# Performance work log

Measured on AMD Instinct MI355X. Metric: run time of the kernel, lower is better.

Reference implementation:

```python
import jax, jax.numpy as jnp
import numpy as np
from jax import lax

B, N, C, HEADS, SR = 2, 4096, 256, 8, 2
HW = 64

def setup_inputs() -> dict:
    key = jax.random.key(0)
    ks = jax.random.split(key, 12)
    s = 0.02
    return {
        "x0": jax.random.normal(ks[0], (B, N, C), jnp.float32),
        "x1": jax.random.normal(ks[1], (B, N, C), jnp.float32),
        "Wq": jax.random.normal(ks[2], (C, C), jnp.float32) * s,
        "Wkv": jax.random.normal(ks[3], (2 * C, C), jnp.float32) * s,
        "Wproj": jax.random.normal(ks[4], (C, C), jnp.float32) * s,
        "bproj": jnp.zeros((C,), jnp.float32),
        "Wsr": jax.random.normal(ks[5], (C, C, SR, SR), jnp.float32) * np.sqrt(2.0 / (SR * SR * C)),
        "bsr": jnp.zeros((C,), jnp.float32),
        "ln_w0": jnp.ones((C,), jnp.float32),
        "ln_b0": jnp.zeros((C,), jnp.float32),
        "ln_w1": jnp.ones((C,), jnp.float32),
        "ln_b1": jnp.zeros((C,), jnp.float32),
        "H": HW,
        "W": HW,
    }

def _layernorm(x, w, b, eps=1e-5):
    mu = jnp.mean(x, axis=-1, keepdims=True)
    var = jnp.mean(jnp.square(x - mu), axis=-1, keepdims=True)
    return (x - mu) * lax.rsqrt(var + eps) * w + b

def _attend(x, ln_w, ln_b, Wq, Wkv, Wproj, bproj, Wsr, bsr, H, W):
    b, n, c = x.shape
    h = HEADS
    d = c // h
    scale = d ** -0.5
    # q: (B, h, N, d)
    q = (x @ Wq.T).reshape(b, n, h, d).transpose(0, 2, 1, 3)
    # spatial reduction: conv k=stride=sr on (B,C,H,W)
    xs = x.transpose(0, 2, 1).reshape(b, c, H, W)
    xs = lax.conv_general_dilated(xs, Wsr, (SR, SR), 'VALID',
                                  dimension_numbers=('NCHW', 'OIHW', 'NCHW'))
    xs = xs + bsr[None, :, None, None]
    m = (H // SR) * (W // SR)
    xs = xs.reshape(b, c, m).transpose(0, 2, 1)  # (B, M, C)
    xs = _layernorm(xs, ln_w, ln_b)
    kv = (xs @ Wkv.T).reshape(b, m, 2, h, d).transpose(2, 0, 3, 1, 4)
    k, v = kv[0], kv[1]  # (B, h, M, d)
    attn = jnp.einsum('bhnd,bhmd->bhnm', q, k) * scale
    attn = jax.nn.softmax(attn, axis=-1)
    out = jnp.einsum('bhnm,bhmd->bhnd', attn, v)
    out = out.transpose(0, 2, 1, 3).reshape(b, n, c)
    return out @ Wproj.T + bproj

def reference(x0, x1, Wq, Wkv, Wproj, bproj, Wsr, bsr, ln_w0, ln_b0, ln_w1, ln_b1, H, W):
    y0 = _attend(x0, ln_w0, ln_b0, Wq, Wkv, Wproj, bproj, Wsr, bsr, H, W)
    y1 = _attend(x1, ln_w1, ln_b1, Wq, Wkv, Wproj, bproj, Wsr, bsr, H, W)
    return (y0, y1)
```

## Files before the change

kernel.cpp:

```cpp
#include <hip/hip_runtime.h>
#include <hip/hip_bf16.h>
#include <cstddef>

typedef __hip_bfloat16 bf16;
typedef __attribute__((ext_vector_type(8))) short bf16x8;
typedef __attribute__((ext_vector_type(4))) float f32x4;
typedef __attribute__((ext_vector_type(4))) short short4v;

__device__ __forceinline__ float b2f(bf16 v) { return __bfloat162float(v); }
__device__ __forceinline__ bf16 f2b(float v) { return __float2bfloat16(v); }

#define MFMA(a, b, c) __builtin_amdgcn_mfma_f32_16x16x32_bf16((a), (b), (c), 0, 0, 0)

#define WQ_OFF   0
#define WKV_OFF  65536
#define WP_OFF   196608
#define WSR_OFF  262144

__global__ __launch_bounds__(256) void cvt_x(
    const float* __restrict__ x0, const float* __restrict__ x1,
    bf16* __restrict__ xb) {
  const int gid = blockIdx.x * 256 + threadIdx.x;
  for (int i = gid; i < 1048576; i += 262144) {
    const float4 v = (i < 524288) ? ((const float4*)x0)[i]
                                  : ((const float4*)x1)[i - 524288];
    union { bf16 h[4]; short4v s; } u;
    u.h[0] = f2b(v.x); u.h[1] = f2b(v.y); u.h[2] = f2b(v.z); u.h[3] = f2b(v.w);
    ((short4v*)xb)[i] = u.s;
  }
}

__global__ __launch_bounds__(256) void cvt_w(
    const float* __restrict__ Wq, const float* __restrict__ Wkv,
    const float* __restrict__ Wp, const float* __restrict__ Wsr,
    bf16* __restrict__ wb) {
  const int gid = blockIdx.x * 256 + threadIdx.x;
  for (int i = gid; i < 524288; i += 131072) {
    float v;
    if (i < WKV_OFF)       v = Wq[i];
    else if (i < WP_OFF)   v = Wkv[i - WKV_OFF];
    else if (i < WSR_OFF)  v = Wp[i - WP_OFF];
    else {
      const int r = i - WSR_OFF;
      const int o = r >> 10, k = r & 1023;
      const int p = k >> 8, c = k & 255;
      v = Wsr[o * 1024 + c * 4 + p];
    }
    wb[i] = f2b(v);
  }
}

#define STAGE_W(W_lds, wgl, ldg)                                             \
  _Pragma("unroll")                                                          \
  for (int u = 0; u < 8; ++u) {                                              \
    const int idx = u * 256 + t;                                             \
    const int wr = idx >> 5;                                                 \
    const int wc = (idx & 31) * 8;                                           \
    *(bf16x8*)&W_lds[wr][wc] = *(const bf16x8*)((wgl) + wr * (ldg) + wc);    \
  }

__global__ __launch_bounds__(256) void qproj_mfma(
    const bf16* __restrict__ xb, const bf16* __restrict__ wb,
    bf16* __restrict__ q) {
  __shared__ bf16 W_lds[64][264];
  const int t = threadIdx.x;
  const int wave = t >> 6, lane = t & 63, quad = lane >> 4, l16 = lane & 15;
  const int row0 = blockIdx.x * 64 + wave * 16;
  const int colh = blockIdx.y * 64;
  STAGE_W(W_lds, wb + WQ_OFF + colh * 256, 256);
  __syncthreads();
  const bf16* ap = xb + (row0 + l16) * 256 + quad * 8;
  f32x4 acc[4];
  #pragma unroll
  for (int j = 0; j < 4; ++j) acc[j] = (f32x4){0.f, 0.f, 0.f, 0.f};
  #pragma unroll
  for (int k0 = 0; k0 < 256; k0 += 32) {
    const bf16x8 af = *(const bf16x8*)(ap + k0);
    #pragma unroll
    for (int j = 0; j < 4; ++j) {
      const bf16x8 wf = *(const bf16x8*)&W_lds[j * 16 + l16][k0 + quad * 8];
      acc[j] = MFMA(af, wf, acc[j]);
    }
  }
  const float scale = 0.17677669529663687f;
  #pragma unroll
  for (int j = 0; j < 4; ++j)
    #pragma unroll
    for (int r = 0; r < 4; ++r)
      q[(row0 + quad * 4 + r) * 256 + colh + j * 16 + l16] =
          f2b(acc[j][r] * scale);
}

__global__ __launch_bounds__(256) void conv_mfma(
    const bf16* __restrict__ xb, const bf16* __restrict__ wb,
    const float* __restrict__ bsr, bf16* __restrict__ xsb) {
  __shared__ bf16 W_lds[64][264];
  const int t = threadIdx.x;
  const int wave = t >> 6, lane = t & 63, quad = lane >> 4, l16 = lane & 15;
  const int row0 = blockIdx.x * 64 + wave * 16;
  const int colh = blockIdx.y * 64;
  const int mrow = row0 + l16;
  const int ab = mrow >> 10;
  const int m = mrow & 1023;
  const int mi_ = m >> 5, mj = m & 31;
  f32x4 acc[4];
  #pragma unroll
  for (int j = 0; j < 4; ++j) acc[j] = (f32x4){0.f, 0.f, 0.f, 0.f};
  for (int p = 0; p < 4; ++p) {
    __syncthreads();
    STAGE_W(W_lds, wb + WSR_OFF + colh * 1024 + p * 256, 1024);
    __syncthreads();
    const int n = (2 * mi_ + (p >> 1)) * 64 + 2 * mj + (p & 1);
    const bf16* ap = xb + (ab * 4096 + n) * 256 + quad * 8;
    #pragma unroll
    for (int c0 = 0; c0 < 256; c0 += 32) {
      const bf16x8 af = *(const bf16x8*)(ap + c0);
      #pragma unroll
      for (int j = 0; j < 4; ++j) {
        const bf16x8 wf = *(const bf16x8*)&W_lds[j * 16 + l16][c0 + quad * 8];
        acc[j] = MFMA(af, wf, acc[j]);
      }
    }
  }
  #pragma unroll
  for (int j = 0; j < 4; ++j) {
    const int col = colh + j * 16 + l16;
    const float bv = bsr[col];
    #pragma unroll
    for (int r = 0; r < 4; ++r)
      xsb[(row0 + quad * 4 + r) * 256 + col] = f2b(acc[j][r] + bv);
  }
}

__global__ __launch_bounds__(256) void ln_kernel(
    bf16* __restrict__ xsb,
    const float* __restrict__ w0, const float* __restrict__ b0,
    const float* __restrict__ w1, const float* __restrict__ b1) {
  const int row = blockIdx.x;
  const int a = row >> 11;
  const int t = threadIdx.x;
  const float v = b2f(xsb[row * 256 + t]);
  __shared__ float red[4], red2[4];
  float s = v;
  #pragma unroll
  for (int off = 32; off >= 1; off >>= 1) s += __shfl_down(s, off, 64);
  if ((t & 63) == 0) red[t >> 6] = s;
  __syncthreads();
  const float mean = (red[0] + red[1] + red[2] + red[3]) * (1.0f / 256.0f);
  const float dv = v - mean;
  float s2 = dv * dv;
  #pragma unroll
  for (int off = 32; off >= 1; off >>= 1) s2 += __shfl_down(s2, off, 64);
  if ((t & 63) == 0) red2[t >> 6] = s2;
  __syncthreads();
  const float var = (red2[0] + red2[1] + red2[2] + red2[3]) * (1.0f / 256.0f);
  const float* w = a ? w1 : w0;
  const float* bbp = a ? b1 : b0;
  xsb[row * 256 + t] = f2b(dv * rsqrtf(var + 1e-5f) * w[t] + bbp[t]);
}

__global__ __launch_bounds__(256) void kv_mfma(
    const bf16* __restrict__ xsb, const bf16* __restrict__ wb,
    bf16* __restrict__ kbuf, bf16* __restrict__ vbuf_t) {
  __shared__ bf16 W_lds[64][264];
  const int t = threadIdx.x;
  const int wave = t >> 6, lane = t & 63, quad = lane >> 4, l16 = lane & 15;
  const int row0 = blockIdx.x * 64 + wave * 16;
  const int colh = blockIdx.y * 64;
  STAGE_W(W_lds, wb + WKV_OFF + colh * 256, 256);
  __syncthreads();
  const bf16* ap = xsb + (row0 + l16) * 256 + quad * 8;
  f32x4 acc[4];
  #pragma unroll
  for (int j = 0; j < 4; ++j) acc[j] = (f32x4){0.f, 0.f, 0.f, 0.f};
  #pragma unroll
  for (int k0 = 0; k0 < 256; k0 += 32) {
    const bf16x8 af = *(const bf16x8*)(ap + k0);
    #pragma unroll
    for (int j = 0; j < 4; ++j) {
      const bf16x8 wf = *(const bf16x8*)&W_lds[j * 16 + l16][k0 + quad * 8];
      acc[j] = MFMA(af, wf, acc[j]);
    }
  }
  #pragma unroll
  for (int j = 0; j < 4; ++j) {
    const int o = colh + j * 16 + l16;
    #pragma unroll
    for (int r = 0; r < 4; ++r) {
      const int row = row0 + quad * 4 + r;
      const int m = row & 1023;
      const bf16 val = f2b(acc[j][r]);
      if (o < 256) {
        const int h = o >> 5, d = o & 31;
        kbuf[((row >> 10) * 8 + h) * 32768 + m * 32 + d] = val;
      } else {
        const int o2 = o - 256;
        const int h = o2 >> 5, d = o2 & 31;
        const int rr = m & 63;
        const int mp = (m & ~63) + (rr & 15) * 4 + (rr >> 4);
        vbuf_t[((row >> 10) * 8 + h) * 32768 + d * 1024 + mp] = val;
      }
    }
  }
}

__global__ __launch_bounds__(256) void attn_mfma(
    const bf16* __restrict__ q, const bf16* __restrict__ kbuf,
    const bf16* __restrict__ vbuf_t, bf16* __restrict__ att) {
  const int abh = blockIdx.y;
  const int ab = abh >> 3;
  const int h = abh & 7;
  const int t = threadIdx.x;
  const int wave = t >> 6, lane = t & 63, quad = lane >> 4, l16 = lane & 15;
  const int qbase = blockIdx.x * 128 + wave * 32;

  __shared__ bf16 KT[2][2048];
  __shared__ bf16 VT[2][2048];
  __shared__ bf16 P_lds[4][2][16][72];

  const bf16* kb = kbuf + abh * 32768;
  const bf16* vb = vbuf_t + abh * 32768;

  const int kg = (t >> 6) * 512 + ((t >> 2) & 15) * 32 + (t & 3) * 8;
  const int vg_row = (t >> 7) * 16 + ((t >> 3) & 15);
  const int vg_col = ((t >> 2) & 1) * 32 + (t & 3) * 8;

  bf16x8 qf[2];
  #pragma unroll
  for (int s = 0; s < 2; ++s)
    qf[s] = *(const bf16x8*)(
        q + (ab * 4096 + qbase + s * 16 + l16) * 256 + h * 32 + quad * 8);

  {
    const bf16x8 kr = *(const bf16x8*)(kb + kg);
    const bf16x8 vr = *(const bf16x8*)(vb + vg_row * 1024 + vg_col);
    *(bf16x8*)&KT[0][t * 8] = kr;
    *(bf16x8*)&VT[0][t * 8] = vr;
  }
  __syncthreads();

  f32x4 o[2][2];
  float lp[2][4];
  #pragma unroll
  for (int s = 0; s < 2; ++s) {
    o[s][0] = (f32x4){0.f, 0.f, 0.f, 0.f};
    o[s][1] = (f32x4){0.f, 0.f, 0.f, 0.f};
    #pragma unroll
    for (int r = 0; r < 4; ++r) lp[s][r] = 0.0f;
  }
  const f32x4 zero = {0.f, 0.f, 0.f, 0.f};

  for (int kt = 0; kt < 16; ++kt) {
    const int cur = kt & 1;
    bf16x8 kr, vr;
    const bool pf = (kt + 1 < 16);
    if (pf) {
      const int nk0 = (kt + 1) * 64;
      kr = *(const bf16x8*)(kb + nk0 * 32 + kg);
      vr = *(const bf16x8*)(vb + vg_row * 1024 + nk0 + vg_col);
    }
    f32x4 S[2][4];
    #pragma unroll
    for (int tt = 0; tt < 4; ++tt) {
      const bf16x8 kf =
          *(const bf16x8*)&KT[cur][(tt * 64 + l16 * 4 + quad) * 8];
      S[0][tt] = MFMA(qf[0], kf, zero);
      S[1][tt] = MFMA(qf[1], kf, zero);
    }
    #pragma unroll
    for (int s = 0; s < 2; ++s) {
      #pragma unroll
      for (int r = 0; r < 4; ++r) {
        const float p0 = __expf(S[s][0][r]);
        const float p1 = __expf(S[s][1][r]);
        const float p2 = __expf(S[s][2][r]);
        const float p3 = __expf(S[s][3][r]);
        lp[s][r] += (p0 + p1) + (p2 + p3);
        const __hip_bfloat162 lo = __float22bfloat162_rn(float2{p0, p1});
        const __hip_bfloat162 hi = __float22bfloat162_rn(float2{p2, p3});
        union { __hip_bfloat162 h2[2]; short4v sv; } u;
        u.h2[0] = lo; u.h2[1] = hi;
        *(short4v*)&P_lds[wave][s][quad * 4 + r][l16 * 4] = u.sv;
      }
    }
    #pragma unroll
    for (int c2 = 0; c2 < 2; ++c2) {
      const bf16x8 pf0 = *(const bf16x8*)&P_lds[wave][0][l16][c2 * 32 + quad * 8];
      const bf16x8 pf1 = *(const bf16x8*)&P_lds[wave][1][l16][c2 * 32 + quad * 8];
      #pragma unroll
      for (int dh = 0; dh < 2; ++dh) {
        const bf16x8 vf = *(const bf16x8*)&VT[cur]
            [(dh * 128 + l16 * 8 + c2 * 4 + quad) * 8];
        o[0][dh] = MFMA(pf0, vf, o[0][dh]);
        o[1][dh] = MFMA(pf1, vf, o[1][dh]);
      }
    }
    if (pf) {
      *(bf16x8*)&KT[cur ^ 1][t * 8] = kr;
      *(bf16x8*)&VT[cur ^ 1][t * 8] = vr;
    }
    __syncthreads();
  }
  #pragma unroll
  for (int s = 0; s < 2; ++s) {
    #pragma unroll
    for (int r = 0; r < 4; ++r) {
      float li = lp[s][r];
      #pragma unroll
      for (int off = 1; off < 16; off <<= 1) li += __shfl_xor(li, off, 16);
      const float inv = 1.0f / li;
      const int qrow = ab * 4096 + qbase + s * 16 + quad * 4 + r;
      bf16* orow = att + qrow * 256 + h * 32;
      orow[l16]      = f2b(o[s][0][r] * inv);
      orow[16 + l16] = f2b(o[s][1][r] * inv);
    }
  }
}

__global__ __launch_bounds__(256) void proj_mfma(
    const bf16* __restrict__ att, const bf16* __restrict__ wb,
    const float* __restrict__ bp, float* __restrict__ outp) {
  __shared__ bf16 W_lds[64][264];
  const int t = threadIdx.x;
  const int wave = t >> 6, lane = t & 63, quad = lane >> 4, l16 = lane & 15;
  const int row0 = blockIdx.x * 64 + wave * 16;
  const int colh = blockIdx.y * 64;
  STAGE_W(W_lds, wb + WP_OFF + colh * 256, 256);
  __syncthreads();
  const bf16* ap = att + (row0 + l16) * 256 + quad * 8;
  f32x4 acc[4];
  #pragma unroll
  for (int j = 0; j < 4; ++j) acc[j] = (f32x4){0.f, 0.f, 0.f, 0.f};
  #pragma unroll
  for (int k0 = 0; k0 < 256; k0 += 32) {
    const bf16x8 af = *(const bf16x8*)(ap + k0);
    #pragma unroll
    for (int j = 0; j < 4; ++j) {
      const bf16x8 wf = *(const bf16x8*)&W_lds[j * 16 + l16][k0 + quad * 8];
      acc[j] = MFMA(af, wf, acc[j]);
    }
  }
  #pragma unroll
  for (int j = 0; j < 4; ++j) {
    const int col = colh + j * 16 + l16;
    const float bv = bp[col];
    #pragma unroll
    for (int r = 0; r < 4; ++r)
      outp[(row0 + quad * 4 + r) * 256 + col] = acc[j][r] + bv;
  }
}

extern "C" void kernel_launch(void* const* d_in, const int* in_sizes, int n_in,
                              void* d_out, int out_size, void* d_ws, size_t ws_size,
                              hipStream_t stream) {
  const float* x0    = (const float*)d_in[0];
  const float* x1    = (const float*)d_in[1];
  const float* Wq    = (const float*)d_in[2];
  const float* Wkv   = (const float*)d_in[3];
  const float* Wproj = (const float*)d_in[4];
  const float* bproj = (const float*)d_in[5];
  const float* Wsr   = (const float*)d_in[6];
  const float* bsr   = (const float*)d_in[7];
  const float* lnw0  = (const float*)d_in[8];
  const float* lnb0  = (const float*)d_in[9];
  const float* lnw1  = (const float*)d_in[10];
  const float* lnb1  = (const float*)d_in[11];

  bf16* q_bf   = (bf16*)d_out;
  bf16* xb     = q_bf + 4194304;
  bf16* att_bf = (bf16*)d_ws;
  bf16* xsb    = att_bf + 4194304;
  bf16* kbuf   = xsb + 1048576;
  bf16* vbuf_t = kbuf + 1048576;
  bf16* wb     = vbuf_t + 1048576;
  float* y     = (float*)d_out;

  const dim3 blk(256);
  cvt_x<<<dim3(1024), blk, 0, stream>>>(x0, x1, xb);
  cvt_w<<<dim3(512), blk, 0, stream>>>(Wq, Wkv, Wproj, Wsr, wb);
  qproj_mfma<<<dim3(256, 4), blk, 0, stream>>>(xb, wb, q_bf);
  conv_mfma<<<dim3(64, 4), blk, 0, stream>>>(xb, wb, bsr, xsb);
  ln_kernel<<<dim3(4096), blk, 0, stream>>>(xsb, lnw0, lnb0, lnw1, lnb1);
  kv_mfma<<<dim3(64, 8), blk, 0, stream>>>(xsb, wb, kbuf, vbuf_t);
  attn_mfma<<<dim3(32, 32), blk, 0, stream>>>(q_bf, kbuf, vbuf_t, att_bf);
  proj_mfma<<<dim3(256, 4), blk, 0, stream>>>(att_bf, wb, bproj, y);
}
```

Measured before the change: 168.7 us.

## Merge prep and projection kernels, fuse LayerNorm into KV GEMM, use exp2

Combines the two conversion kernels into one launch and runs the Q projection and the strided conv as separate block ranges of a single launch. LayerNorm is folded into the KV projection: each lane loads its full row, computes mean and variance with a single-pass sum and sum of squares, and normalises in registers, which removes the standalone LN kernel and its round trip through xsb. The q scale now includes log2(e), so softmax can use the hardware exp2 instruction. This cuts three launches and one memory pass. The cost is that LN is recomputed by every column block of the KV GEMM, and the single-pass variance is slightly less numerically stable.

```diff
diff --git a/kernel.cpp b/kernel.cpp
--- a/kernel.cpp
+++ b/kernel.cpp
@@ -17,36 +17,37 @@
 #define WP_OFF   196608
 #define WSR_OFF  262144
 
-__global__ __launch_bounds__(256) void cvt_x(
+__global__ __launch_bounds__(256) void prep_cvt(
     const float* __restrict__ x0, const float* __restrict__ x1,
-    bf16* __restrict__ xb) {
-  const int gid = blockIdx.x * 256 + threadIdx.x;
-  for (int i = gid; i < 1048576; i += 262144) {
-    const float4 v = (i < 524288) ? ((const float4*)x0)[i]
-                                  : ((const float4*)x1)[i - 524288];
-    union { bf16 h[4]; short4v s; } u;
-    u.h[0] = f2b(v.x); u.h[1] = f2b(v.y); u.h[2] = f2b(v.z); u.h[3] = f2b(v.w);
-    ((short4v*)xb)[i] = u.s;
-  }
-}
-
-__global__ __launch_bounds__(256) void cvt_w(
+    bf16* __restrict__ xb,
     const float* __restrict__ Wq, const float* __restrict__ Wkv,
     const float* __restrict__ Wp, const float* __restrict__ Wsr,
     bf16* __restrict__ wb) {
-  const int gid = blockIdx.x * 256 + threadIdx.x;
-  for (int i = gid; i < 524288; i += 131072) {
-    float v;
-    if (i < WKV_OFF)       v = Wq[i];
-    else if (i < WP_OFF)   v = Wkv[i - WKV_OFF];
-    else if (i < WSR_OFF)  v = Wp[i - WP_OFF];
-    else {
-      const int r = i - WSR_OFF;
-      const int o = r >> 10, k = r & 1023;
-      const int p = k >> 8, c = k & 255;
-      v = Wsr[o * 1024 + c * 4 + p];
-    }
-    wb[i] = f2b(v);
+  const int t = threadIdx.x;
+  if (blockIdx.x < 1024) {
+    const int gid = blockIdx.x * 256 + t;
+    for (int i = gid; i < 1048576; i += 262144) {
+      const float4 v = (i < 524288) ? ((const float4*)x0)[i]
+                                    : ((const float4*)x1)[i - 524288];
+      union { bf16 h[4]; short4v s; } u;
+      u.h[0] = f2b(v.x); u.h[1] = f2b(v.y); u.h[2] = f2b(v.z); u.h[3] = f2b(v.w);
+      ((short4v*)xb)[i] = u.s;
+    }
+  } else {
+    const int gid = (blockIdx.x - 1024) * 256 + t;
+    for (int i = gid; i < 524288; i += 131072) {
+      float v;
+      if (i < WKV_OFF)       v = Wq[i];
+      else if (i < WP_OFF)   v = Wkv[i - WKV_OFF];
+      else if (i < WSR_OFF)  v = Wp[i - WP_OFF];
+      else {
+        const int r = i - WSR_OFF;
+        const int o = r >> 10, k = r & 1023;
+        const int p = k >> 8, c = k & 255;
+        v = Wsr[o * 1024 + c * 4 + p];
+      }
+      wb[i] = f2b(v);
+    }
   }
 }
 
@@ -59,127 +60,131 @@
     *(bf16x8*)&W_lds[wr][wc] = *(const bf16x8*)((wgl) + wr * (ldg) + wc);    \
   }
 
-__global__ __launch_bounds__(256) void qproj_mfma(
+__global__ __launch_bounds__(256) void qc_mfma(
     const bf16* __restrict__ xb, const bf16* __restrict__ wb,
-    bf16* __restrict__ q) {
+    const float* __restrict__ bsr, bf16* __restrict__ q,
+    bf16* __restrict__ xsb) {
   __shared__ bf16 W_lds[64][264];
+  const int t = threadIdx.x;
+  const int wave = t >> 6, lane = t & 63, quad = lane >> 4, l16 = lane & 15;
+  const int colh = blockIdx.y * 64;
+
+  if (blockIdx.x < 256) {
+    const int row0 = blockIdx.x * 64 + wave * 16;
+    STAGE_W(W_lds, wb + WQ_OFF + colh * 256, 256);
+    __syncthreads();
+    const bf16* ap = xb + (row0 + l16) * 256 + quad * 8;
+    f32x4 acc[4];
+    #pragma unroll
+    for (int j = 0; j < 4; ++j) acc[j] = (f32x4){0.f, 0.f, 0.f, 0.f};
+    #pragma unroll
+    for (int k0 = 0; k0 < 256; k0 += 32) {
+      const bf16x8 af = *(const bf16x8*)(ap + k0);
+      #pragma unroll
+      for (int j = 0; j < 4; ++j) {
+        const bf16x8 wf = *(const bf16x8*)&W_lds[j * 16 + l16][k0 + quad * 8];
+        acc[j] = MFMA(af, wf, acc[j]);
+      }
+    }
+    const float scale = 0.2550348572f;
+    #pragma unroll
+    for (int j = 0; j < 4; ++j)
+      #pragma unroll
+      for (int r = 0; r < 4; ++r)
+        q[(row0 + quad * 4 + r) * 256 + colh + j * 16 + l16] =
+            f2b(acc[j][r] * scale);
+  } else {
+    const int bx = blockIdx.x - 256;
+    const int row0 = bx * 64 + wave * 16;
+    const int mrow = row0 + l16;
+    const int ab = mrow >> 10;
+    const int m = mrow & 1023;
+    const int mi_ = m >> 5, mj = m & 31;
+    f32x4 acc[4];
+    #pragma unroll
+    for (int j = 0; j < 4; ++j) acc[j] = (f32x4){0.f, 0.f, 0.f, 0.f};
+    for (int p = 0; p < 4; ++p) {
+      __syncthreads();
+      STAGE_W(W_lds, wb + WSR_OFF + colh * 1024 + p * 256, 1024);
+      __syncthreads();
+      const int n = (2 * mi_ + (p >> 1)) * 64 + 2 * mj + (p & 1);
+      const bf16* ap = xb + (ab * 4096 + n) * 256 + quad * 8;
+      #pragma unroll
+      for (int c0 = 0; c0 < 256; c0 += 32) {
+        const bf16x8 af = *(const bf16x8*)(ap + c0);
+        #pragma unroll
+        for (int j = 0; j < 4; ++j) {
+          const bf16x8 wf = *(const bf16x8*)&W_lds[j * 16 + l16][c0 + quad * 8];
+          acc[j] = MFMA(af, wf, acc[j]);
+        }
+      }
+    }
+    #pragma unroll
+    for (int j = 0; j < 4; ++j) {
+      const int col = colh + j * 16 + l16;
+      const float bv = bsr[col];
+      #pragma unroll
+      for (int r = 0; r < 4; ++r)
+        xsb[(row0 + quad * 4 + r) * 256 + col] = f2b(acc[j][r] + bv);
+    }
+  }
+}
+
+__global__ __launch_bounds__(256) void kvln_mfma(
+    const bf16* __restrict__ xsb, const bf16* __restrict__ wb,
+    const float* __restrict__ w0, const float* __restrict__ b0,
+    const float* __restrict__ w1, const float* __restrict__ b1,
+    bf16* __restrict__ kbuf, bf16* __restrict__ vbuf_t) {
+  __shared__ bf16 W_lds[64][264];
+  __shared__ float lnw[256], lnb[256];
   const int t = threadIdx.x;
   const int wave = t >> 6, lane = t & 63, quad = lane >> 4, l16 = lane & 15;
   const int row0 = blockIdx.x * 64 + wave * 16;
   const int colh = blockIdx.y * 64;
-  STAGE_W(W_lds, wb + WQ_OFF + colh * 256, 256);
-  __syncthreads();
-  const bf16* ap = xb + (row0 + l16) * 256 + quad * 8;
-  f32x4 acc[4];
-  #pragma unroll
-  for (int j = 0; j < 4; ++j) acc[j] = (f32x4){0.f, 0.f, 0.f, 0.f};
-  #pragma unroll
-  for (int k0 = 0; k0 < 256; k0 += 32) {
-    const bf16x8 af = *(const bf16x8*)(ap + k0);
-    #pragma unroll
-    for (int j = 0; j < 4; ++j) {
-      const bf16x8 wf = *(const bf16x8*)&W_lds[j * 16 + l16][k0 + quad * 8];
-      acc[j] = MFMA(af, wf, acc[j]);
-    }
-  }
-  const float scale = 0.17677669529663687f;
-  #pragma unroll
-  for (int j = 0; j < 4; ++j)
-    #pragma unroll
-    for (int r = 0; r < 4; ++r)
-      q[(row0 + quad * 4 + r) * 256 + colh + j * 16 + l16] =
-          f2b(acc[j][r] * scale);
-}
-
-__global__ __launch_bounds__(256) void conv_mfma(
-    const bf16* __restrict__ xb, const bf16* __restrict__ wb,
-    const float* __restrict__ bsr, bf16* __restrict__ xsb) {
-  __shared__ bf16 W_lds[64][264];
-  const int t = threadIdx.x;
-  const int wave = t >> 6, lane = t & 63, quad = lane >> 4, l16 = lane & 15;
-  const int row0 = blockIdx.x * 64 + wave * 16;
-  const int colh = blockIdx.y * 64;
-  const int mrow = row0 + l16;
-  const int ab = mrow >> 10;
-  const int m = mrow & 1023;
-  const int mi_ = m >> 5, mj = m & 31;
-  f32x4 acc[4];
-  #pragma unroll
-  for (int j = 0; j < 4; ++j) acc[j] = (f32x4){0.f, 0.f, 0.f, 0.f};
-  for (int p = 0; p < 4; ++p) {
-    __syncthreads();
-    STAGE_W(W_lds, wb + WSR_OFF + colh * 1024 + p * 256, 1024);
-    __syncthreads();
-    const int n = (2 * mi_ + (p >> 1)) * 64 + 2 * mj + (p & 1);
-    const bf16* ap = xb + (ab * 4096 + n) * 256 + quad * 8;
-    #pragma unroll
-    for (int c0 = 0; c0 < 256; c0 += 32) {
-      const bf16x8 af = *(const bf16x8*)(ap + c0);
-      #pragma unroll
-      for (int j = 0; j < 4; ++j) {
-        const bf16x8 wf = *(const bf16x8*)&W_lds[j * 16 + l16][c0 + quad * 8];
-        acc[j] = MFMA(af, wf, acc[j]);
-      }
-    }
-  }
-  #pragma unroll
-  for (int j = 0; j < 4; ++j) {
-    const int col = colh + j * 16 + l16;
-    const float bv = bsr[col];
-    #pragma unroll
-    for (int r = 0; r < 4; ++r)
-      xsb[(row0 + quad * 4 + r) * 256 + col] = f2b(acc[j][r] + bv);
-  }
-}
-
-__global__ __launch_bounds__(256) void ln_kernel(
-    bf16* __restrict__ xsb,
-    const float* __restrict__ w0, const float* __restrict__ b0,
-    const float* __restrict__ w1, const float* __restrict__ b1) {
-  const int row = blockIdx.x;
-  const int a = row >> 11;
-  const int t = threadIdx.x;
-  const float v = b2f(xsb[row * 256 + t]);
-  __shared__ float red[4], red2[4];
-  float s = v;
-  #pragma unroll
-  for (int off = 32; off >= 1; off >>= 1) s += __shfl_down(s, off, 64);
-  if ((t & 63) == 0) red[t >> 6] = s;
-  __syncthreads();
-  const float mean = (red[0] + red[1] + red[2] + red[3]) * (1.0f / 256.0f);
-  const float dv = v - mean;
-  float s2 = dv * dv;
-  #pragma unroll
-  for (int off = 32; off >= 1; off >>= 1) s2 += __shfl_down(s2, off, 64);
-  if ((t & 63) == 0) red2[t >> 6] = s2;
-  __syncthreads();
-  const float var = (red2[0] + red2[1] + red2[2] + red2[3]) * (1.0f / 256.0f);
-  const float* w = a ? w1 : w0;
-  const float* bbp = a ? b1 : b0;
-  xsb[row * 256 + t] = f2b(dv * rsqrtf(var + 1e-5f) * w[t] + bbp[t]);
-}
-
-__global__ __launch_bounds__(256) void kv_mfma(
-    const bf16* __restrict__ xsb, const bf16* __restrict__ wb,
-    bf16* __restrict__ kbuf, bf16* __restrict__ vbuf_t) {
-  __shared__ bf16 W_lds[64][264];
-  const int t = threadIdx.x;
-  const int wave = t >> 6, lane = t & 63, quad = lane >> 4, l16 = lane & 15;
-  const int row0 = blockIdx.x * 64 + wave * 16;
-  const int colh = blockIdx.y * 64;
+  const int a = (blockIdx.x * 64) >> 11;
+  lnw[t] = a ? w1[t] : w0[t];
+  lnb[t] = a ? b1[t] : b0[t];
   STAGE_W(W_lds, wb + WKV_OFF + colh * 256, 256);
   __syncthreads();
+
   const bf16* ap = xsb + (row0 + l16) * 256 + quad * 8;
+  bf16x8 af[8];
+  float sum = 0.f, ss = 0.f;
+  #pragma unroll
+  for (int i = 0; i < 8; ++i) {
+    af[i] = *(const bf16x8*)(ap + i * 32);
+    #pragma unroll
+    for (int e = 0; e < 8; ++e) {
+      const float x = b2f(((bf16*)&af[i])[e]);
+      sum += x; ss += x * x;
+    }
+  }
+  sum += __shfl_xor(sum, 16, 64); sum += __shfl_xor(sum, 32, 64);
+  ss  += __shfl_xor(ss, 16, 64);  ss  += __shfl_xor(ss, 32, 64);
+  const float mu = sum * (1.0f / 256.0f);
+  const float var = ss * (1.0f / 256.0f) - mu * mu;
+  const float rstd = rsqrtf(var + 1e-5f);
+  #pragma unroll
+  for (int i = 0; i < 8; ++i) {
+    const int cb = i * 32 + quad * 8;
+    union { bf16 h[8]; bf16x8 v; } u;
+    #pragma unroll
+    for (int e = 0; e < 8; ++e) {
+      const float x = b2f(((bf16*)&af[i])[e]);
+      u.h[e] = f2b((x - mu) * rstd * lnw[cb + e] + lnb[cb + e]);
+    }
+    af[i] = u.v;
+  }
+
   f32x4 acc[4];
   #pragma unroll
   for (int j = 0; j < 4; ++j) acc[j] = (f32x4){0.f, 0.f, 0.f, 0.f};
   #pragma unroll
-  for (int k0 = 0; k0 < 256; k0 += 32) {
-    const bf16x8 af = *(const bf16x8*)(ap + k0);
+  for (int i = 0; i < 8; ++i) {
     #pragma unroll
     for (int j = 0; j < 4; ++j) {
-      const bf16x8 wf = *(const bf16x8*)&W_lds[j * 16 + l16][k0 + quad * 8];
-      acc[j] = MFMA(af, wf, acc[j]);
+      const bf16x8 wf = *(const bf16x8*)&W_lds[j * 16 + l16][i * 32 + quad * 8];
+      acc[j] = MFMA(af[i], wf, acc[j]);
     }
   }
   #pragma unroll
@@ -271,10 +276,10 @@
     for (int s = 0; s < 2; ++s) {
       #pragma unroll
       for (int r = 0; r < 4; ++r) {
-        const float p0 = __expf(S[s][0][r]);
-        const float p1 = __expf(S[s][1][r]);
-        const float p2 = __expf(S[s][2][r]);
-        const float p3 = __expf(S[s][3][r]);
+        const float p0 = __builtin_amdgcn_exp2f(S[s][0][r]);
+        const float p1 = __builtin_amdgcn_exp2f(S[s][1][r]);
+        const float p2 = __builtin_amdgcn_exp2f(S[s][2][r]);
+        const float p3 = __builtin_amdgcn_exp2f(S[s][3][r]);
         lp[s][r] += (p0 + p1) + (p2 + p3);
         const __hip_bfloat162 lo = __float22bfloat162_rn(float2{p0, p1});
         const __hip_bfloat162 hi = __float22bfloat162_rn(float2{p2, p3});
@@ -376,12 +381,10 @@
   float* y     = (float*)d_out;
 
   const dim3 blk(256);
-  cvt_x<<<dim3(1024), blk, 0, stream>>>(x0, x1, xb);
-  cvt_w<<<dim3(512), blk, 0, stream>>>(Wq, Wkv, Wproj, Wsr, wb);
-  qproj_mfma<<<dim3(256, 4), blk, 0, stream>>>(xb, wb, q_bf);
-  conv_mfma<<<dim3(64, 4), blk, 0, stream>>>(xb, wb, bsr, xsb);
-  ln_kernel<<<dim3(4096), blk, 0, stream>>>(xsb, lnw0, lnb0, lnw1, lnb1);
-  kv_mfma<<<dim3(64, 8), blk, 0, stream>>>(xsb, wb, kbuf, vbuf_t);
+  prep_cvt<<<dim3(1536), blk, 0, stream>>>(x0, x1, xb, Wq, Wkv, Wproj, Wsr, wb);
+  qc_mfma<<<dim3(320, 4), blk, 0, stream>>>(xb, wb, bsr, q_bf, xsb);
+  kvln_mfma<<<dim3(64, 8), blk, 0, stream>>>(xsb, wb, lnw0, lnb0, lnw1, lnb1,
+                                             kbuf, vbuf_t);
   attn_mfma<<<dim3(32, 32), blk, 0, stream>>>(q_bf, kbuf, vbuf_t, att_bf);
   proj_mfma<<<dim3(256, 4), blk, 0, stream>>>(att_bf, wb, bproj, y);
 }
```

After: 160.8 us. -4.7%, faster.
